# Kernel optimization log

Hardware: AMD Instinct MI355X
Metric: run time of the kernel (lower is better)

Reference implementation:

```python
import jax, jax.numpy as jnp
import numpy as np

NDIM = 1024
NHEAD = 16
HEAD_DIM = NDIM // NHEAD


def setup_inputs() -> dict:
    key = jax.random.key(0)
    ks = jax.random.split(key, 12)
    B, L, C = 2, 2048, NDIM
    s = 0.02
    return {
        "q": jax.random.normal(ks[0], (B, L, C), jnp.float32),
        "k": jax.random.normal(ks[1], (B, L, C), jnp.float32),
        "v": jax.random.normal(ks[2], (B, L, C), jnp.float32),
        "Wq": jax.random.normal(ks[3], (C, C), jnp.float32) * s,
        "bq": jax.random.normal(ks[4], (C,), jnp.float32) * s,
        "Wk": jax.random.normal(ks[5], (C, C), jnp.float32) * s,
        "bk": jax.random.normal(ks[6], (C,), jnp.float32) * s,
        "Wv": jax.random.normal(ks[7], (C, C), jnp.float32) * s,
        "bv": jax.random.normal(ks[8], (C,), jnp.float32) * s,
        "Wo": jax.random.normal(ks[9], (C, C), jnp.float32) * s,
        "bo": jax.random.normal(ks[10], (C,), jnp.float32) * s,
    }


def reference(q, k, v, Wq, bq, Wk, bk, Wv, bv, Wo, bo):
    B, Lq, C = q.shape
    H, D = NHEAD, HEAD_DIM
    # projections, then split heads: (B, H, L, D)
    qh = (q @ Wq + bq).reshape(B, Lq, H, D).transpose(0, 2, 1, 3)
    kh = (k @ Wk + bk).reshape(B, k.shape[1], H, D).transpose(0, 2, 1, 3)
    vh = (v @ Wv + bv).reshape(B, v.shape[1], H, D).transpose(0, 2, 1, 3)
    scale = 1.0 / jnp.sqrt(jnp.asarray(D, qh.dtype))
    att = jnp.einsum("bhqd,bhkd->bhqk", qh, kh) * scale  # (B,H,Lq,Lk)
    att = jax.nn.softmax(att, axis=-1)  # dropout p=0.0 -> identity
    y = jnp.einsum("bhqk,bhkd->bhqd", att, vh)
    y = y.transpose(0, 2, 1, 3).reshape(B, Lq, C)
    return y @ Wo + bo
```

## Files before the change

kernel.cpp:

```cpp
#include <hip/hip_runtime.h>
#include <math.h>

#define BATCH 2
#define SEQ   2048
#define CDIM  1024
#define NHEAD 16
#define HDIM  64
#define TOKS  (BATCH * SEQ)

typedef __bf16 bf16x8 __attribute__((ext_vector_type(8)));
typedef __bf16 bf16x2 __attribute__((ext_vector_type(2)));
typedef float  f32x4  __attribute__((ext_vector_type(4)));

#define MFMA16(a, b, c) __builtin_amdgcn_mfma_f32_16x16x32_bf16(a, b, c, 0, 0, 0)

#define QSCALE 0.1803368801111204f

__device__ __forceinline__ void gload_lds16(const __bf16* g, __bf16* l) {
    __builtin_amdgcn_global_load_lds(
        (const __attribute__((address_space(1))) unsigned int*)g,
        (__attribute__((address_space(3))) unsigned int*)l, 16, 0, 0);
}

__global__ __launch_bounds__(256) void prep_kernel(
    const float* __restrict__ q, const float* __restrict__ k, const float* __restrict__ v,
    __bf16* __restrict__ qo, __bf16* __restrict__ ko, __bf16* __restrict__ vo,
    const float* __restrict__ W0, const float* __restrict__ W1,
    const float* __restrict__ W2, const float* __restrict__ W3,
    __bf16* __restrict__ T0, __bf16* __restrict__ T1,
    __bf16* __restrict__ T2, __bf16* __restrict__ T3)
{
    __shared__ __bf16 Ts[64][72];
    const int bx = blockIdx.x;
    const int tid = threadIdx.x;

    if (bx < 6144) {
        const int t = bx >> 11;
        const size_t i = ((size_t)(bx & 2047) * 256 + tid) * 8;
        const float* s = t == 0 ? q : (t == 1 ? k : v);
        __bf16* d = t == 0 ? qo : (t == 1 ? ko : vo);
        const float4 x = *(const float4*)&s[i];
        const float4 y = *(const float4*)&s[i + 4];
        bf16x8 o;
        o[0] = (__bf16)x.x; o[1] = (__bf16)x.y; o[2] = (__bf16)x.z; o[3] = (__bf16)x.w;
        o[4] = (__bf16)y.x; o[5] = (__bf16)y.y; o[6] = (__bf16)y.z; o[7] = (__bf16)y.w;
        *(bf16x8*)&d[i] = o;
        return;
    }

    const int t  = bx - 6144;
    const int z  = t >> 8;
    const int ry = (t & 255) >> 4;
    const int rx = t & 15;
    const float* W = z == 0 ? W0 : z == 1 ? W1 : z == 2 ? W2 : W3;
    __bf16* T = z == 0 ? T0 : z == 1 ? T1 : z == 2 ? T2 : T3;
    const int rb = ry * 64, cb = rx * 64;
    const int r = tid >> 4;
    const int c4 = (tid & 15) * 4;
#pragma unroll
    for (int p = 0; p < 4; p++) {
        const int rr = p * 16 + r;
        const float4 w4 = *(const float4*)&W[(size_t)(rb + rr) * CDIM + cb + c4];
        Ts[c4 + 0][rr] = (__bf16)w4.x;
        Ts[c4 + 1][rr] = (__bf16)w4.y;
        Ts[c4 + 2][rr] = (__bf16)w4.z;
        Ts[c4 + 3][rr] = (__bf16)w4.w;
    }
    __syncthreads();
    const int n = tid >> 2;
    const int k16 = (tid & 3) * 16;
    *(bf16x8*)&T[(size_t)(cb + n) * CDIM + rb + k16]     = *(const bf16x8*)&Ts[n][k16];
    *(bf16x8*)&T[(size_t)(cb + n) * CDIM + rb + k16 + 8] = *(const bf16x8*)&Ts[n][k16 + 8];
}

__global__ __launch_bounds__(256) void qkv_gemm_kernel(
    const __bf16* __restrict__ qb, const __bf16* __restrict__ kb,
    const __bf16* __restrict__ vb,
    const __bf16* __restrict__ Wqt, const __bf16* __restrict__ Wkt,
    const __bf16* __restrict__ Wvt,
    const float* __restrict__ bq, const float* __restrict__ bk,
    const float* __restrict__ bv,
    __bf16* __restrict__ Qh, __bf16* __restrict__ Kh, __bf16* __restrict__ Vht)
{
    __shared__ __bf16 As[128 * 32];
    __shared__ __bf16 Bs[128 * 32];

    const int z = blockIdx.z;
    const __bf16* A    = z == 0 ? qb : z == 1 ? kb : Wvt;
    const __bf16* Bt   = z == 0 ? Wqt : z == 1 ? Wkt : vb;
    const float*  bias = z == 0 ? bq : z == 1 ? bk : bv;

    const int tid  = threadIdx.x;
    const int w    = tid >> 6;
    const int lane = tid & 63;
    const int quad = lane >> 4;
    const int c    = lane & 15;
    const int wm   = w >> 1;
    const int wn   = w & 1;
    const int rowBase = (z == 2 ? blockIdx.x : blockIdx.y) * 128;
    const int colBase = (z == 2 ? blockIdx.y : blockIdx.x) * 128;

    const int sr = lane >> 2;
    const int sk = (lane & 3) * 8;

    f32x4 acc[4][4];
#pragma unroll
    for (int i = 0; i < 4; i++)
#pragma unroll
        for (int j = 0; j < 4; j++) acc[i][j] = (f32x4){0, 0, 0, 0};

    for (int k0 = 0; k0 < CDIM; k0 += 32) {
#pragma unroll
        for (int j = 0; j < 2; j++) {
            const int r0 = (w * 2 + j) * 16;
            gload_lds16(A  + (size_t)(rowBase + r0 + sr) * CDIM + k0 + sk, &As[r0 * 32]);
            gload_lds16(Bt + (size_t)(colBase + r0 + sr) * CDIM + k0 + sk, &Bs[r0 * 32]);
        }
        __syncthreads();

        bf16x8 af[4], bf[4];
#pragma unroll
        for (int i = 0; i < 4; i++) {
            af[i] = *(const bf16x8*)&As[(wm * 64 + i * 16 + c) * 32 + quad * 8];
            bf[i] = *(const bf16x8*)&Bs[(wn * 64 + i * 16 + c) * 32 + quad * 8];
        }
#pragma unroll
        for (int mi = 0; mi < 4; mi++)
#pragma unroll
            for (int ni = 0; ni < 4; ni++)
                acc[mi][ni] = MFMA16(af[mi], bf[ni], acc[mi][ni]);
        __syncthreads();
    }

#pragma unroll
    for (int mi = 0; mi < 4; mi++) {
#pragma unroll
        for (int ni = 0; ni < 4; ni++) {
            const int col = colBase + wn * 64 + ni * 16 + c;
#pragma unroll
            for (int r = 0; r < 4; r++) {
                const int row = rowBase + wm * 64 + mi * 16 + quad * 4 + r;
                const float val = acc[mi][ni][r];
                if (z == 2) {
                    const int col2 = (col & ~31) | (((col & 15) << 1) | ((col >> 4) & 1));
                    Vht[(size_t)row * TOKS + col2] = (__bf16)(val + bias[row]);
                } else {
                    const int b = row >> 11, l = row & 2047;
                    const int h = col >> 6,  d = col & 63;
                    const float s = (z == 0) ? QSCALE : 1.0f;
                    __bf16* outp = (z == 0) ? Qh : Kh;
                    outp[((((size_t)b * NHEAD + h) * SEQ) + l) * HDIM + d] =
                        (__bf16)((val + bias[col]) * s);
                }
            }
        }
    }
}

__global__ __launch_bounds__(256) void out_gemm_kernel(
    const __bf16* __restrict__ A, const __bf16* __restrict__ Bt,
    const float* __restrict__ bias, float* __restrict__ out)
{
    __shared__ __bf16 As[128 * 32];
    __shared__ __bf16 Bs[64 * 32];

    const int tid  = threadIdx.x;
    const int w    = tid >> 6;
    const int lane = tid & 63;
    const int quad = lane >> 4;
    const int c    = lane & 15;
    const int wm   = w >> 1;
    const int wn   = w & 1;
    const int rowBase = blockIdx.y * 128;
    const int colBase = blockIdx.x * 64;
    const int sr = lane >> 2;
    const int sk = (lane & 3) * 8;

    f32x4 acc[4][2];
#pragma unroll
    for (int i = 0; i < 4; i++)
#pragma unroll
        for (int j = 0; j < 2; j++) acc[i][j] = (f32x4){0, 0, 0, 0};

    for (int k0 = 0; k0 < CDIM; k0 += 32) {
#pragma unroll
        for (int j = 0; j < 2; j++) {
            const int r0 = (w * 2 + j) * 16;
            gload_lds16(A + (size_t)(rowBase + r0 + sr) * CDIM + k0 + sk, &As[r0 * 32]);
        }
        gload_lds16(Bt + (size_t)(colBase + w * 16 + sr) * CDIM + k0 + sk, &Bs[w * 16 * 32]);
        __syncthreads();

        bf16x8 af[4], bf[2];
#pragma unroll
        for (int i = 0; i < 4; i++)
            af[i] = *(const bf16x8*)&As[(wm * 64 + i * 16 + c) * 32 + quad * 8];
#pragma unroll
        for (int i = 0; i < 2; i++)
            bf[i] = *(const bf16x8*)&Bs[(wn * 32 + i * 16 + c) * 32 + quad * 8];
#pragma unroll
        for (int mi = 0; mi < 4; mi++)
#pragma unroll
            for (int ni = 0; ni < 2; ni++)
                acc[mi][ni] = MFMA16(af[mi], bf[ni], acc[mi][ni]);
        __syncthreads();
    }

#pragma unroll
    for (int mi = 0; mi < 4; mi++) {
#pragma unroll
        for (int ni = 0; ni < 2; ni++) {
            const int col = colBase + wn * 32 + ni * 16 + c;
#pragma unroll
            for (int r = 0; r < 4; r++) {
                const int row = rowBase + wm * 64 + mi * 16 + quad * 4 + r;
                out[(size_t)row * CDIM + col] = acc[mi][ni][r] + bias[col];
            }
        }
    }
}

__global__ __launch_bounds__(256) void attn_v5_kernel(
    const __bf16* __restrict__ Qh, const __bf16* __restrict__ Kh,
    const __bf16* __restrict__ Vht, __bf16* __restrict__ Y)
{
    __shared__ __align__(16) __bf16 Ks[2][32][72];
    __shared__ __align__(16) __bf16 Vt[2][64][48];
    __shared__ __align__(16) unsigned int Pf[4][2][16][36];

    const int tid  = threadIdx.x;
    const int w    = tid >> 6;
    const int lane = tid & 63;
    const int quad = lane >> 4;
    const int c    = lane & 15;
    const int bh   = blockIdx.x;
    const int b    = bh >> 4;
    const int h    = bh & 15;
    const int qbase = blockIdx.y * 128 + w * 32;

    const __bf16* Qg = Qh + (size_t)bh * SEQ * HDIM;
    const __bf16* Kg = Kh + (size_t)bh * SEQ * HDIM;
    const __bf16* Vg = Vht + (size_t)(h * HDIM) * TOKS + (size_t)b * SEQ;

    bf16x8 qf[2][2];
#pragma unroll
    for (int g = 0; g < 2; g++) {
        qf[g][0] = *(const bf16x8*)&Qg[(size_t)(qbase + g * 16 + c) * HDIM + quad * 8];
        qf[g][1] = *(const bf16x8*)&Qg[(size_t)(qbase + g * 16 + c) * HDIM + 32 + quad * 8];
    }

    bf16x8 ones;
#pragma unroll
    for (int j = 0; j < 8; j++) ones[j] = (__bf16)1.0f;

    f32x4 O[2][4];
    f32x4 L[2];
#pragma unroll
    for (int g = 0; g < 2; g++) {
        L[g] = (f32x4){0, 0, 0, 0};
#pragma unroll
        for (int i = 0; i < 4; i++) O[g][i] = (f32x4){0, 0, 0, 0};
    }

    const int krow = tid >> 3, kcol = (tid & 7) * 8;
    const int vrow = tid >> 2, vcol = (tid & 3) * 8;

    {
        const bf16x8 k0 = *(const bf16x8*)&Kg[(size_t)krow * HDIM + kcol];
        const bf16x8 v0 = *(const bf16x8*)&Vg[(size_t)vrow * TOKS + vcol];
        *(bf16x8*)&Ks[0][krow][kcol] = k0;
        *(bf16x8*)&Vt[0][vrow][vcol] = v0;
    }
    __syncthreads();

    int buf = 0;
    for (int t0 = 0; t0 < SEQ; t0 += 32) {
        const int tn = t0 + 32;
        bf16x8 kpre, vpre;
        if (tn < SEQ) {
            kpre = *(const bf16x8*)&Kg[(size_t)(tn + krow) * HDIM + kcol];
            vpre = *(const bf16x8*)&Vg[(size_t)vrow * TOKS + tn + vcol];
        }

        const bf16x8 k00 = *(const bf16x8*)&Ks[buf][c][quad * 8];
        const bf16x8 k01 = *(const bf16x8*)&Ks[buf][c][32 + quad * 8];
        const bf16x8 k10 = *(const bf16x8*)&Ks[buf][16 + c][quad * 8];
        const bf16x8 k11 = *(const bf16x8*)&Ks[buf][16 + c][32 + quad * 8];
        const bf16x8 v0 = *(const bf16x8*)&Vt[buf][c][quad * 8];
        const bf16x8 v1 = *(const bf16x8*)&Vt[buf][16 + c][quad * 8];
        const bf16x8 v2 = *(const bf16x8*)&Vt[buf][32 + c][quad * 8];
        const bf16x8 v3 = *(const bf16x8*)&Vt[buf][48 + c][quad * 8];

#pragma unroll
        for (int g = 0; g < 2; g++) {
            f32x4 s0 = {0, 0, 0, 0}, s1 = {0, 0, 0, 0};
            s0 = MFMA16(qf[g][0], k00, s0);
            s0 = MFMA16(qf[g][1], k01, s0);
            s1 = MFMA16(qf[g][0], k10, s1);
            s1 = MFMA16(qf[g][1], k11, s1);
#pragma unroll
            for (int r = 0; r < 4; r++) {
                union { bf16x2 v; unsigned int u; } pk;
                pk.v[0] = (__bf16)__builtin_amdgcn_exp2f(s0[r]);
                pk.v[1] = (__bf16)__builtin_amdgcn_exp2f(s1[r]);
                Pf[w][g][quad * 4 + r][c] = pk.u;
            }
            const bf16x8 pf = *(const bf16x8*)&Pf[w][g][c][quad * 4];
            L[g]    = MFMA16(pf, ones, L[g]);
            O[g][0] = MFMA16(pf, v0, O[g][0]);
            O[g][1] = MFMA16(pf, v1, O[g][1]);
            O[g][2] = MFMA16(pf, v2, O[g][2]);
            O[g][3] = MFMA16(pf, v3, O[g][3]);
        }

        if (tn < SEQ) {
            *(bf16x8*)&Ks[buf ^ 1][krow][kcol] = kpre;
            *(bf16x8*)&Vt[buf ^ 1][vrow][vcol] = vpre;
        }
        __syncthreads();
        buf ^= 1;
    }

    __bf16* Yb = Y + (size_t)b * SEQ * CDIM;
#pragma unroll
    for (int g = 0; g < 2; g++) {
#pragma unroll
        for (int r = 0; r < 4; r++) {
            const float inv = 1.0f / L[g][r];
            const int l = qbase + g * 16 + quad * 4 + r;
            __bf16* yp = Yb + (size_t)l * CDIM + h * HDIM + c;
            yp[0]  = (__bf16)(O[g][0][r] * inv);
            yp[16] = (__bf16)(O[g][1][r] * inv);
            yp[32] = (__bf16)(O[g][2][r] * inv);
            yp[48] = (__bf16)(O[g][3][r] * inv);
        }
    }
}


extern "C" void kernel_launch(void* const* d_in, const int* in_sizes, int n_in,
                              void* d_out, int out_size, void* d_ws, size_t ws_size,
                              hipStream_t stream)
{
    const float* q  = (const float*)d_in[0];
    const float* k  = (const float*)d_in[1];
    const float* v  = (const float*)d_in[2];
    const float* Wq = (const float*)d_in[3];
    const float* bq = (const float*)d_in[4];
    const float* Wk = (const float*)d_in[5];
    const float* bk = (const float*)d_in[6];
    const float* Wv = (const float*)d_in[7];
    const float* bv = (const float*)d_in[8];
    const float* Wo = (const float*)d_in[9];
    const float* bo = (const float*)d_in[10];
    float* out = (float*)d_out;

    const size_t MAT = (size_t)TOKS * CDIM;
    const size_t WN  = (size_t)CDIM * CDIM;

    __bf16* p   = (__bf16*)d_ws;
    __bf16* qb  = p; p += MAT;
    __bf16* kb  = p; p += MAT;
    __bf16* vb  = p; p += MAT;
    __bf16* Wqt = p; p += WN;
    __bf16* Wkt = p; p += WN;
    __bf16* Wvt = p; p += WN;
    __bf16* Wot = p; p += WN;
    __bf16* Qh  = p; p += MAT;
    __bf16* Kh  = p; p += MAT;
    __bf16* Vht = p; p += MAT;
    __bf16* Yb  = qb;

    prep_kernel<<<dim3(7168), dim3(256), 0, stream>>>(
        q, k, v, qb, kb, vb, Wq, Wk, Wv, Wo, Wqt, Wkt, Wvt, Wot);

    qkv_gemm_kernel<<<dim3(8, 32, 3), dim3(256), 0, stream>>>(
        qb, kb, vb, Wqt, Wkt, Wvt, bq, bk, bv, Qh, Kh, Vht);

    attn_v5_kernel<<<dim3(BATCH * NHEAD, SEQ / 128), dim3(256), 0, stream>>>(Qh, Kh, Vht, Yb);

    out_gemm_kernel<<<dim3(16, 32), dim3(256), 0, stream>>>(Yb, Wot, bo, out);
}
```

Before: 231.4 us.

## Use 512-thread blocks in projection GEMMs and remap block order for XCD locality

Both projection GEMM kernels now launch 512 threads (8 waves) per block, and each wave computes half as many output rows, which cuts per-wave accumulator registers. Each loader wave issues one global-to-LDS load per matrix per k-step instead of two. Block indices are remapped so consecutive hardware block IDs, which are dealt round-robin across the 8 XCDs, land on neighbouring tiles and can share L2. The tile size and LDS footprint stay the same, but there are more waves per CU at the cost of more threads sharing each barrier and a smaller per-wave MFMA batch between syncs.

After: 225.4 us. 2.6% less time.

```diff
diff --git a/kernel.cpp b/kernel.cpp
--- a/kernel.cpp
+++ b/kernel.cpp
@@ -73,7 +73,7 @@
     *(bf16x8*)&T[(size_t)(cb + n) * CDIM + rb + k16 + 8] = *(const bf16x8*)&Ts[n][k16 + 8];
 }
 
-__global__ __launch_bounds__(256) void qkv_gemm_kernel(
+__global__ __launch_bounds__(512, 6) void qkv_gemm_kernel(
     const __bf16* __restrict__ qb, const __bf16* __restrict__ kb,
     const __bf16* __restrict__ vb,
     const __bf16* __restrict__ Wqt, const __bf16* __restrict__ Wkt,
@@ -85,7 +85,12 @@
     __shared__ __bf16 As[128 * 32];
     __shared__ __bf16 Bs[128 * 32];
 
-    const int z = blockIdx.z;
+    const int lin = blockIdx.x + (blockIdx.y << 3) + (blockIdx.z << 8);
+    const int nl  = (lin & 7) * 96 + (lin >> 3);
+    const int bx  = nl & 7;
+    const int by  = (nl >> 3) & 31;
+    const int z   = nl >> 8;
+
     const __bf16* A    = z == 0 ? qb : z == 1 ? kb : Wvt;
     const __bf16* Bt   = z == 0 ? Wqt : z == 1 ? Wkt : vb;
     const float*  bias = z == 0 ? bq : z == 1 ? bk : bv;
@@ -97,35 +102,37 @@
     const int c    = lane & 15;
     const int wm   = w >> 1;
     const int wn   = w & 1;
-    const int rowBase = (z == 2 ? blockIdx.x : blockIdx.y) * 128;
-    const int colBase = (z == 2 ? blockIdx.y : blockIdx.x) * 128;
+    const int rowBase = (z == 2 ? bx : by) * 128;
+    const int colBase = (z == 2 ? by : bx) * 128;
 
     const int sr = lane >> 2;
     const int sk = (lane & 3) * 8;
 
-    f32x4 acc[4][4];
-#pragma unroll
-    for (int i = 0; i < 4; i++)
+    f32x4 acc[2][4];
+#pragma unroll
+    for (int i = 0; i < 2; i++)
 #pragma unroll
         for (int j = 0; j < 4; j++) acc[i][j] = (f32x4){0, 0, 0, 0};
 
+    const __bf16* srcA = A  + (size_t)(rowBase + w * 16 + sr) * CDIM + sk;
+    const __bf16* srcB = Bt + (size_t)(colBase + w * 16 + sr) * CDIM + sk;
+    __bf16* dstA = &As[w * 16 * 32];
+    __bf16* dstB = &Bs[w * 16 * 32];
+
     for (int k0 = 0; k0 < CDIM; k0 += 32) {
-#pragma unroll
-        for (int j = 0; j < 2; j++) {
-            const int r0 = (w * 2 + j) * 16;
-            gload_lds16(A  + (size_t)(rowBase + r0 + sr) * CDIM + k0 + sk, &As[r0 * 32]);
-            gload_lds16(Bt + (size_t)(colBase + r0 + sr) * CDIM + k0 + sk, &Bs[r0 * 32]);
-        }
-        __syncthreads();
-
-        bf16x8 af[4], bf[4];
-#pragma unroll
-        for (int i = 0; i < 4; i++) {
-            af[i] = *(const bf16x8*)&As[(wm * 64 + i * 16 + c) * 32 + quad * 8];
+        gload_lds16(srcA + k0, dstA);
+        gload_lds16(srcB + k0, dstB);
+        __syncthreads();
+
+        bf16x8 af[2], bf[4];
+#pragma unroll
+        for (int i = 0; i < 2; i++)
+            af[i] = *(const bf16x8*)&As[(wm * 32 + i * 16 + c) * 32 + quad * 8];
+#pragma unroll
+        for (int i = 0; i < 4; i++)
             bf[i] = *(const bf16x8*)&Bs[(wn * 64 + i * 16 + c) * 32 + quad * 8];
-        }
-#pragma unroll
-        for (int mi = 0; mi < 4; mi++)
+#pragma unroll
+        for (int mi = 0; mi < 2; mi++)
 #pragma unroll
             for (int ni = 0; ni < 4; ni++)
                 acc[mi][ni] = MFMA16(af[mi], bf[ni], acc[mi][ni]);
@@ -133,13 +140,13 @@
     }
 
 #pragma unroll
-    for (int mi = 0; mi < 4; mi++) {
+    for (int mi = 0; mi < 2; mi++) {
 #pragma unroll
         for (int ni = 0; ni < 4; ni++) {
             const int col = colBase + wn * 64 + ni * 16 + c;
 #pragma unroll
             for (int r = 0; r < 4; r++) {
-                const int row = rowBase + wm * 64 + mi * 16 + quad * 4 + r;
+                const int row = rowBase + wm * 32 + mi * 16 + quad * 4 + r;
                 const float val = acc[mi][ni][r];
                 if (z == 2) {
                     const int col2 = (col & ~31) | (((col & 15) << 1) | ((col >> 4) & 1));
@@ -157,12 +164,17 @@
     }
 }
 
-__global__ __launch_bounds__(256) void out_gemm_kernel(
+__global__ __launch_bounds__(512, 4) void out_gemm_kernel(
     const __bf16* __restrict__ A, const __bf16* __restrict__ Bt,
     const float* __restrict__ bias, float* __restrict__ out)
 {
     __shared__ __bf16 As[128 * 32];
     __shared__ __bf16 Bs[64 * 32];
+
+    const int lin = blockIdx.x + (blockIdx.y << 4);
+    const int nl  = (lin & 7) * 64 + (lin >> 3);
+    const int bx  = nl & 15;
+    const int by  = nl >> 4;
 
     const int tid  = threadIdx.x;
     const int w    = tid >> 6;
@@ -171,35 +183,36 @@
     const int c    = lane & 15;
     const int wm   = w >> 1;
     const int wn   = w & 1;
-    const int rowBase = blockIdx.y * 128;
-    const int colBase = blockIdx.x * 64;
+    const int rowBase = by * 128;
+    const int colBase = bx * 64;
     const int sr = lane >> 2;
     const int sk = (lane & 3) * 8;
 
-    f32x4 acc[4][2];
-#pragma unroll
-    for (int i = 0; i < 4; i++)
+    f32x4 acc[2][2];
+#pragma unroll
+    for (int i = 0; i < 2; i++)
 #pragma unroll
         for (int j = 0; j < 2; j++) acc[i][j] = (f32x4){0, 0, 0, 0};
 
+    const __bf16* srcA = A + (size_t)(rowBase + w * 16 + sr) * CDIM + sk;
+    const __bf16* srcB = Bt + (size_t)(colBase + (w & 3) * 16 + sr) * CDIM + sk;
+    __bf16* dstA = &As[w * 16 * 32];
+    __bf16* dstB = &Bs[(w & 3) * 16 * 32];
+
     for (int k0 = 0; k0 < CDIM; k0 += 32) {
-#pragma unroll
-        for (int j = 0; j < 2; j++) {
-            const int r0 = (w * 2 + j) * 16;
-            gload_lds16(A + (size_t)(rowBase + r0 + sr) * CDIM + k0 + sk, &As[r0 * 32]);
-        }
-        gload_lds16(Bt + (size_t)(colBase + w * 16 + sr) * CDIM + k0 + sk, &Bs[w * 16 * 32]);
-        __syncthreads();
-
-        bf16x8 af[4], bf[2];
-#pragma unroll
-        for (int i = 0; i < 4; i++)
-            af[i] = *(const bf16x8*)&As[(wm * 64 + i * 16 + c) * 32 + quad * 8];
+        gload_lds16(srcA + k0, dstA);
+        if (w < 4) gload_lds16(srcB + k0, dstB);
+        __syncthreads();
+
+        bf16x8 af[2], bf[2];
+#pragma unroll
+        for (int i = 0; i < 2; i++)
+            af[i] = *(const bf16x8*)&As[(wm * 32 + i * 16 + c) * 32 + quad * 8];
 #pragma unroll
         for (int i = 0; i < 2; i++)
             bf[i] = *(const bf16x8*)&Bs[(wn * 32 + i * 16 + c) * 32 + quad * 8];
 #pragma unroll
-        for (int mi = 0; mi < 4; mi++)
+        for (int mi = 0; mi < 2; mi++)
 #pragma unroll
             for (int ni = 0; ni < 2; ni++)
                 acc[mi][ni] = MFMA16(af[mi], bf[ni], acc[mi][ni]);
@@ -207,13 +220,13 @@
     }
 
 #pragma unroll
-    for (int mi = 0; mi < 4; mi++) {
+    for (int mi = 0; mi < 2; mi++) {
 #pragma unroll
         for (int ni = 0; ni < 2; ni++) {
             const int col = colBase + wn * 32 + ni * 16 + c;
 #pragma unroll
             for (int r = 0; r < 4; r++) {
-                const int row = rowBase + wm * 64 + mi * 16 + quad * 4 + r;
+                const int row = rowBase + wm * 32 + mi * 16 + quad * 4 + r;
                 out[(size_t)row * CDIM + col] = acc[mi][ni][r] + bias[col];
             }
         }
@@ -374,10 +387,10 @@
     prep_kernel<<<dim3(7168), dim3(256), 0, stream>>>(
         q, k, v, qb, kb, vb, Wq, Wk, Wv, Wo, Wqt, Wkt, Wvt, Wot);
 
-    qkv_gemm_kernel<<<dim3(8, 32, 3), dim3(256), 0, stream>>>(
+    qkv_gemm_kernel<<<dim3(8, 32, 3), dim3(512), 0, stream>>>(
         qb, kb, vb, Wqt, Wkt, Wvt, bq, bk, bv, Qh, Kh, Vht);
 
     attn_v5_kernel<<<dim3(BATCH * NHEAD, SEQ / 128), dim3(256), 0, stream>>>(Qh, Kh, Vht, Yb);
 
-    out_gemm_kernel<<<dim3(16, 32), dim3(256), 0, stream>>>(Yb, Wot, bo, out);
-}
+    out_gemm_kernel<<<dim3(16, 32), dim3(512), 0, stream>>>(Yb, Wot, bo, out);
+}
```
